# Performance work log

Hardware: AMD Instinct MI355X
Metric: run time of the kernel (lower is better)

The kernel has to match this reference:

```python
import jax, jax.numpy as jnp
import numpy as np

B, T, E, H = 2, 384, 768, 12
HD = E // H  # 64


def setup_inputs() -> dict:
    key = jax.random.key(0)
    ks = jax.random.split(key, 12)
    s = 0.02  # init scale
    inp = {
        "hidden_states": jax.random.normal(ks[0], (B, T, E), dtype=jnp.float32),
        # Linear weights stored as [in, out] so forward is x @ W + b
        "Wq": jax.random.normal(ks[1], (E, E), dtype=jnp.float32) * s,
        "bq": jnp.zeros((E,), dtype=jnp.float32),
        "Wk": jax.random.normal(ks[2], (E, E), dtype=jnp.float32) * s,
        "bk": jnp.zeros((E,), dtype=jnp.float32),
        "Wv": jax.random.normal(ks[3], (E, E), dtype=jnp.float32) * s,
        "bv": jnp.zeros((E,), dtype=jnp.float32),
        "Wo": jax.random.normal(ks[4], (E, E), dtype=jnp.float32) * s,
        "bo": jnp.zeros((E,), dtype=jnp.float32),
        # score_proj: Linear(head_dim, 1)
        "w_score": jax.random.normal(ks[5], (HD,), dtype=jnp.float32) * s,
        "b_score": jnp.zeros((1,), dtype=jnp.float32),
    }
    return inp


def reference(hidden_states, Wq, bq, Wk, bk, Wv, bv, Wo, bo, w_score, b_score):
    bsz, tgt_len, embed_dim = hidden_states.shape
    num_heads = H
    head_dim = embed_dim // num_heads

    def shape_heads(x):  # [B, L, E] -> [B, H, L, hd]
        return x.reshape(bsz, -1, num_heads, head_dim).transpose(0, 2, 1, 3)

    q = shape_heads(hidden_states @ Wq + bq)  # [B,H,T,hd]
    k = shape_heads(hidden_states @ Wk + bk)  # [B,H,S,hd]
    v = shape_heads(hidden_states @ Wv + bv)  # [B,H,S,hd]

    # additive (Bahdanau) score: score_proj(tanh(q_t + k_s)) -> [B,H,T,S]
    feat = jnp.tanh(q[:, :, :, None, :] + k[:, :, None, :, :])  # [B,H,T,S,hd]
    score = jnp.einsum("bhtsd,d->bhts", feat, w_score) + b_score[0]

    p_attn = jax.nn.softmax(score, axis=-1)                      # [B,H,T,S]
    attn = jnp.einsum("bhts,bhsd->bhtd", p_attn, v)              # [B,H,T,hd]

    attn = attn.transpose(0, 2, 1, 3).reshape(bsz, tgt_len, embed_dim)
    return attn @ Wo + bo
```

## Files before the change

kernel.cpp:

```cpp
#include <hip/hip_runtime.h>

#define Bc 2
#define Tc 384
#define Ec 768
#define Hc 12
#define HDc 64
#define TTc 8
#define SCc 64
#define NCHUNK (Tc / SCc)

typedef __attribute__((ext_vector_type(8))) short short8;
typedef __attribute__((ext_vector_type(4))) float f32x4;

#define CCONST 2.8853900817779268f

__device__ __forceinline__ float fexp2(float x) { return __builtin_amdgcn_exp2f(x); }
__device__ __forceinline__ float frcp(float x)  { return __builtin_amdgcn_rcpf(x); }

__device__ __forceinline__ unsigned short bf16_rne(float x) {
    unsigned u = __float_as_uint(x);
    u += 0x7fffu + ((u >> 16) & 1u);
    return (unsigned short)(u >> 16);
}
__device__ __forceinline__ float bf16_to_f(unsigned short h) {
    return __uint_as_float(((unsigned)h) << 16);
}

__global__ __launch_bounds__(256) void prep_kernel(
    const float* __restrict__ hs,
    const float* __restrict__ Wq, const float* __restrict__ Wk,
    const float* __restrict__ Wv, const float* __restrict__ Wo,
    unsigned short* __restrict__ hs_hi,
    unsigned short* __restrict__ wt_hi, unsigned short* __restrict__ wt_lo)
{
    const int tid = threadIdx.x;
    int id = blockIdx.x;
    if (id < 144) {
        int base = id * 4096 + tid * 16;
#pragma unroll
        for (int i = 0; i < 4; ++i) {
            float4 x = *reinterpret_cast<const float4*>(&hs[base + i * 4]);
            ushort4 hv;
            hv.x = bf16_rne(x.x);
            hv.y = bf16_rne(x.y);
            hv.z = bf16_rne(x.z);
            hv.w = bf16_rne(x.w);
            *reinterpret_cast<ushort4*>(&hs_hi[base + i * 4]) = hv;
        }
    } else {
        id -= 144;
        const int w = id / 144, t = id % 144;
        const int tr = t / 12, tc2 = t % 12;
        const float* W = (w == 0) ? Wq : (w == 1) ? Wk : (w == 2) ? Wv : Wo;
        unsigned short* TH = wt_hi + (size_t)w * Ec * Ec;
        unsigned short* TL = wt_lo + (size_t)w * Ec * Ec;

        __shared__ float tile[64][68];
        const int r = tid >> 2, c0 = (tid & 3) * 16;
#pragma unroll
        for (int i = 0; i < 4; ++i)
            *reinterpret_cast<float4*>(&tile[r][c0 + i * 4]) =
                *reinterpret_cast<const float4*>(&W[(tr * 64 + r) * Ec + tc2 * 64 + c0 + i * 4]);
        __syncthreads();
        const int n = tid >> 2, k0 = (tid & 3) * 4;
#pragma unroll
        for (int i = 0; i < 4; ++i) {
            int k = k0 + i * 16;
            float v0 = tile[k + 0][n], v1 = tile[k + 1][n];
            float v2 = tile[k + 2][n], v3 = tile[k + 3][n];
            ushort4 hv;
            hv.x = bf16_rne(v0);
            hv.y = bf16_rne(v1);
            hv.z = bf16_rne(v2);
            hv.w = bf16_rne(v3);
            size_t off = (size_t)(tc2 * 64 + n) * Ec + tr * 64 + k;
            *reinterpret_cast<ushort4*>(&TH[off]) = hv;
            if (w == 3) {
                ushort4 lv;
                lv.x = bf16_rne(v0 - bf16_to_f(hv.x));
                lv.y = bf16_rne(v1 - bf16_to_f(hv.y));
                lv.z = bf16_rne(v2 - bf16_to_f(hv.z));
                lv.w = bf16_rne(v3 - bf16_to_f(hv.w));
                *reinterpret_cast<ushort4*>(&TL[off]) = lv;
            }
        }
    }
}

__global__ __launch_bounds__(256) void gemm_qkv(
    const unsigned short* __restrict__ Ahi,
    const unsigned short* __restrict__ Bh0,
    const unsigned short* __restrict__ Bh1,
    const unsigned short* __restrict__ Bh2,
    const float* __restrict__ b0, const float* __restrict__ b1, const float* __restrict__ b2,
    float* __restrict__ C0, float* __restrict__ C1,
    unsigned short* __restrict__ Vt)
{
    const int z = blockIdx.z;
    const unsigned short* Bhi = (z == 0) ? Bh0 : (z == 1) ? Bh1 : Bh2;
    const float* bias = (z == 0) ? b0 : (z == 1) ? b1 : b2;

    __shared__ __align__(16) short sAh[64][72], sBh[64][72];

    const int tid = threadIdx.x;
    const int m0 = blockIdx.y * 64, n0 = blockIdx.x * 64;
    const int wave = tid >> 6, lane = tid & 63;
    const int wm = (wave >> 1) * 32, wn = (wave & 1) * 32;
    const int fr = lane & 15, fk = (lane >> 4) * 8;
    const int sr = tid >> 3, sg = (tid & 7) * 8;

    f32x4 zero = {0.f, 0.f, 0.f, 0.f};
    f32x4 acc[2][2];
    acc[0][0] = zero; acc[0][1] = zero; acc[1][0] = zero; acc[1][1] = zero;

    for (int kc = 0; kc < Ec; kc += 64) {
        int4 a0 = *reinterpret_cast<const int4*>(&Ahi[(size_t)(m0 + sr) * Ec + kc + sg]);
        int4 a1 = *reinterpret_cast<const int4*>(&Ahi[(size_t)(m0 + sr + 32) * Ec + kc + sg]);
        int4 w0 = *reinterpret_cast<const int4*>(&Bhi[(size_t)(n0 + sr) * Ec + kc + sg]);
        int4 w1 = *reinterpret_cast<const int4*>(&Bhi[(size_t)(n0 + sr + 32) * Ec + kc + sg]);
        __syncthreads();
        *reinterpret_cast<int4*>(&sAh[sr][sg])      = a0;
        *reinterpret_cast<int4*>(&sAh[sr + 32][sg]) = a1;
        *reinterpret_cast<int4*>(&sBh[sr][sg])      = w0;
        *reinterpret_cast<int4*>(&sBh[sr + 32][sg]) = w1;
        __syncthreads();

#pragma unroll
        for (int ks = 0; ks < 64; ks += 32) {
            short8 ah[2], bh[2];
#pragma unroll
            for (int mi = 0; mi < 2; ++mi)
                ah[mi] = *reinterpret_cast<const short8*>(&sAh[wm + mi * 16 + fr][ks + fk]);
#pragma unroll
            for (int ni = 0; ni < 2; ++ni)
                bh[ni] = *reinterpret_cast<const short8*>(&sBh[wn + ni * 16 + fr][ks + fk]);
#pragma unroll
            for (int mi = 0; mi < 2; ++mi)
#pragma unroll
                for (int ni = 0; ni < 2; ++ni)
                    acc[mi][ni] = __builtin_amdgcn_mfma_f32_16x16x32_bf16(ah[mi], bh[ni], acc[mi][ni], 0, 0, 0);
        }
        __syncthreads();
    }

    const int rbase = (lane >> 4) * 4;
#pragma unroll
    for (int ni = 0; ni < 2; ++ni) {
        const int cn = n0 + wn + ni * 16 + fr;
        const float bsv = bias[cn];
#pragma unroll
        for (int mi = 0; mi < 2; ++mi) {
            const int rm = m0 + wm + mi * 16 + rbase;
            if (z == 2) {
                const int bb = rm / Tc, ss = rm % Tc;
                const int hh = cn >> 6, dd = cn & 63;
                ushort4 pk;
                pk.x = bf16_rne(acc[mi][ni][0] + bsv);
                pk.y = bf16_rne(acc[mi][ni][1] + bsv);
                pk.z = bf16_rne(acc[mi][ni][2] + bsv);
                pk.w = bf16_rne(acc[mi][ni][3] + bsv);
                *reinterpret_cast<ushort4*>(
                    &Vt[((size_t)(bb * Hc + hh) * HDc + dd) * Tc + ss]) = pk;
            } else {
                float* C = (z == 0) ? C0 : C1;
#pragma unroll
                for (int rr = 0; rr < 4; ++rr)
                    C[(size_t)(rm + rr) * Ec + cn] = fexp2((acc[mi][ni][rr] + bsv) * CCONST);
            }
        }
    }
}

__global__ __launch_bounds__(256) void gemm_out(
    const unsigned short* __restrict__ Ahi, const unsigned short* __restrict__ Alo,
    const unsigned short* __restrict__ Bhi, const unsigned short* __restrict__ Blo,
    const float* __restrict__ bias_p,
    float* __restrict__ C0)
{
    __shared__ __align__(16) short sAh[64][72], sAl[64][72], sBh[64][72], sBl[64][72];

    const int tid = threadIdx.x;
    const int m0 = blockIdx.y * 64, n0 = blockIdx.x * 64;
    const int wave = tid >> 6, lane = tid & 63;
    const int wm = (wave >> 1) * 32, wn = (wave & 1) * 32;
    const int fr = lane & 15, fk = (lane >> 4) * 8;
    const int sr = tid >> 3, sg = (tid & 7) * 8;

    f32x4 zero = {0.f, 0.f, 0.f, 0.f};
    f32x4 acc[2][2];
    acc[0][0] = zero; acc[0][1] = zero; acc[1][0] = zero; acc[1][1] = zero;

    for (int kc = 0; kc < Ec; kc += 64) {
        int4 a0 = *reinterpret_cast<const int4*>(&Ahi[(size_t)(m0 + sr) * Ec + kc + sg]);
        int4 a1 = *reinterpret_cast<const int4*>(&Ahi[(size_t)(m0 + sr + 32) * Ec + kc + sg]);
        int4 a2 = *reinterpret_cast<const int4*>(&Alo[(size_t)(m0 + sr) * Ec + kc + sg]);
        int4 a3 = *reinterpret_cast<const int4*>(&Alo[(size_t)(m0 + sr + 32) * Ec + kc + sg]);
        int4 w0 = *reinterpret_cast<const int4*>(&Bhi[(size_t)(n0 + sr) * Ec + kc + sg]);
        int4 w1 = *reinterpret_cast<const int4*>(&Bhi[(size_t)(n0 + sr + 32) * Ec + kc + sg]);
        int4 w2 = *reinterpret_cast<const int4*>(&Blo[(size_t)(n0 + sr) * Ec + kc + sg]);
        int4 w3 = *reinterpret_cast<const int4*>(&Blo[(size_t)(n0 + sr + 32) * Ec + kc + sg]);
        __syncthreads();
        *reinterpret_cast<int4*>(&sAh[sr][sg])      = a0;
        *reinterpret_cast<int4*>(&sAh[sr + 32][sg]) = a1;
        *reinterpret_cast<int4*>(&sAl[sr][sg])      = a2;
        *reinterpret_cast<int4*>(&sAl[sr + 32][sg]) = a3;
        *reinterpret_cast<int4*>(&sBh[sr][sg])      = w0;
        *reinterpret_cast<int4*>(&sBh[sr + 32][sg]) = w1;
        *reinterpret_cast<int4*>(&sBl[sr][sg])      = w2;
        *reinterpret_cast<int4*>(&sBl[sr + 32][sg]) = w3;
        __syncthreads();

#pragma unroll
        for (int ks = 0; ks < 64; ks += 32) {
            short8 ah[2], al[2], bh[2], bl[2];
#pragma unroll
            for (int mi = 0; mi < 2; ++mi) {
                ah[mi] = *reinterpret_cast<const short8*>(&sAh[wm + mi * 16 + fr][ks + fk]);
                al[mi] = *reinterpret_cast<const short8*>(&sAl[wm + mi * 16 + fr][ks + fk]);
            }
#pragma unroll
            for (int ni = 0; ni < 2; ++ni) {
                bh[ni] = *reinterpret_cast<const short8*>(&sBh[wn + ni * 16 + fr][ks + fk]);
                bl[ni] = *reinterpret_cast<const short8*>(&sBl[wn + ni * 16 + fr][ks + fk]);
            }
#pragma unroll
            for (int mi = 0; mi < 2; ++mi)
#pragma unroll
                for (int ni = 0; ni < 2; ++ni) {
                    acc[mi][ni] = __builtin_amdgcn_mfma_f32_16x16x32_bf16(ah[mi], bh[ni], acc[mi][ni], 0, 0, 0);
                    acc[mi][ni] = __builtin_amdgcn_mfma_f32_16x16x32_bf16(ah[mi], bl[ni], acc[mi][ni], 0, 0, 0);
                    acc[mi][ni] = __builtin_amdgcn_mfma_f32_16x16x32_bf16(al[mi], bh[ni], acc[mi][ni], 0, 0, 0);
                }
        }
        __syncthreads();
    }

    const int rbase = (lane >> 4) * 4;
#pragma unroll
    for (int ni = 0; ni < 2; ++ni) {
        const int cn = n0 + wn + ni * 16 + fr;
        const float bsv = bias_p[cn];
#pragma unroll
        for (int mi = 0; mi < 2; ++mi) {
            const int rm = m0 + wm + mi * 16 + rbase;
#pragma unroll
            for (int rr = 0; rr < 4; ++rr)
                C0[(size_t)(rm + rr) * Ec + cn] = acc[mi][ni][rr] + bsv;
        }
    }
}

__global__ __launch_bounds__(256) void score_softmax_kernel(
    const float* __restrict__ EQ, const float* __restrict__ EK,
    const float* __restrict__ w_score,
    unsigned short* __restrict__ Pg, float* __restrict__ Rinv)
{
    const int bh = blockIdx.x;
    const int b = bh / Hc, h = bh % Hc;
    const int t0 = blockIdx.y * TTc;
    const int tid = threadIdx.x;
    const int wave = tid >> 6, lane = tid & 63;

    __shared__ float qs[TTc][HDc];
    __shared__ float kv[SCc][HDc + 4];
    __shared__ float wsh[HDc];

    {
        int r = tid >> 5, d2 = (tid & 31) << 1;
        float2 qv = *reinterpret_cast<const float2*>(
            &EQ[(size_t)(b * Tc + t0 + r) * Ec + h * HDc + d2]);
        qs[r][d2] = qv.x;
        qs[r][d2 + 1] = qv.y;
        if (tid < HDc) wsh[tid] = w_score[tid];
    }
    __syncthreads();

    const int ta = wave, tb = wave + 4;
    unsigned short* dstA = &Pg[((size_t)bh * Tc + t0 + ta) * Tc + lane];
    unsigned short* dstB = &Pg[((size_t)bh * Tc + t0 + tb) * Tc + lane];

    float sum0 = 0.f, sum1 = 0.f;

    for (int c = 0; c < NCHUNK; ++c) {
        const int s0 = c * SCc;
        if (c > 0) __syncthreads();
#pragma unroll
        for (int i = 0; i < 4; ++i) {
            int id = i * 256 + tid;
            int srr = id >> 4, d4 = (id & 15) << 2;
            float4 kvv = *reinterpret_cast<const float4*>(
                &EK[(size_t)(b * Tc + s0 + srr) * Ec + h * HDc + d4]);
            *reinterpret_cast<float4*>(&kv[srr][d4]) = kvv;
        }
        __syncthreads();
        float a0 = 0.f, a1 = 0.f;
#pragma unroll
        for (int d4 = 0; d4 < HDc; d4 += 4) {
            float4 w4 = *reinterpret_cast<const float4*>(&wsh[d4]);
            float4 qa = *reinterpret_cast<const float4*>(&qs[ta][d4]);
            float4 qb = *reinterpret_cast<const float4*>(&qs[tb][d4]);
            float4 k4 = *reinterpret_cast<const float4*>(&kv[lane][d4]);
            a0 = fmaf(w4.x, frcp(fmaf(qa.x, k4.x, 1.f)), a0);
            a0 = fmaf(w4.y, frcp(fmaf(qa.y, k4.y, 1.f)), a0);
            a0 = fmaf(w4.z, frcp(fmaf(qa.z, k4.z, 1.f)), a0);
            a0 = fmaf(w4.w, frcp(fmaf(qa.w, k4.w, 1.f)), a0);
            a1 = fmaf(w4.x, frcp(fmaf(qb.x, k4.x, 1.f)), a1);
            a1 = fmaf(w4.y, frcp(fmaf(qb.y, k4.y, 1.f)), a1);
            a1 = fmaf(w4.z, frcp(fmaf(qb.z, k4.z, 1.f)), a1);
            a1 = fmaf(w4.w, frcp(fmaf(qb.w, k4.w, 1.f)), a1);
        }
        float p0 = fexp2(-a0 * CCONST);
        float p1 = fexp2(-a1 * CCONST);
        dstA[s0] = bf16_rne(p0);
        dstB[s0] = bf16_rne(p1);
        sum0 += p0;
        sum1 += p1;
    }

#pragma unroll
    for (int off = 32; off > 0; off >>= 1) {
        sum0 += __shfl_xor(sum0, off, 64);
        sum1 += __shfl_xor(sum1, off, 64);
    }
    if (lane == 0) {
        Rinv[(size_t)bh * Tc + t0 + ta] = frcp(sum0);
        Rinv[(size_t)bh * Tc + t0 + tb] = frcp(sum1);
    }
}

__global__ __launch_bounds__(256) void pv_mfma(
    const unsigned short* __restrict__ Pg, const unsigned short* __restrict__ Vt,
    const float* __restrict__ Rinv,
    unsigned short* __restrict__ Ohi, unsigned short* __restrict__ Olo)
{
    const int bh = blockIdx.x;
    const int b = bh / Hc, h = bh % Hc;
    const int tt = blockIdx.y;
    const int tid = threadIdx.x;
    const int wave = tid >> 6, lane = tid & 63;
    const int fr = lane & 15, fk = (lane >> 4) * 8;

    const unsigned short* Pbase = Pg + ((size_t)bh * Tc + tt * 64 + wave * 16 + fr) * Tc + fk;
    const unsigned short* Vbase = Vt + (size_t)bh * HDc * Tc + fk;

    f32x4 zero = {0.f, 0.f, 0.f, 0.f};
    f32x4 acc[4];
    acc[0] = zero; acc[1] = zero; acc[2] = zero; acc[3] = zero;

    for (int ks = 0; ks < Tc; ks += 32) {
        short8 af = *reinterpret_cast<const short8*>(Pbase + ks);
#pragma unroll
        for (int ni = 0; ni < 4; ++ni) {
            short8 bf = *reinterpret_cast<const short8*>(
                Vbase + (size_t)(ni * 16 + fr) * Tc + ks);
            acc[ni] = __builtin_amdgcn_mfma_f32_16x16x32_bf16(af, bf, acc[ni], 0, 0, 0);
        }
    }

    const int rbase = (lane >> 4) * 4;
    float rv[4];
#pragma unroll
    for (int rr = 0; rr < 4; ++rr)
        rv[rr] = Rinv[(size_t)bh * Tc + tt * 64 + wave * 16 + rbase + rr];

#pragma unroll
    for (int ni = 0; ni < 4; ++ni) {
#pragma unroll
        for (int rr = 0; rr < 4; ++rr) {
            int t_out = tt * 64 + wave * 16 + rbase + rr;
            float x = acc[ni][rr] * rv[rr];
            unsigned short hb = bf16_rne(x);
            unsigned short lb = bf16_rne(x - bf16_to_f(hb));
            size_t idx = (size_t)(b * Tc + t_out) * Ec + h * HDc + ni * 16 + fr;
            Ohi[idx] = hb;
            Olo[idx] = lb;
        }
    }
}

extern "C" void kernel_launch(void* const* d_in, const int* in_sizes, int n_in,
                              void* d_out, int out_size, void* d_ws, size_t ws_size,
                              hipStream_t stream) {
    const float* hs  = (const float*)d_in[0];
    const float* Wq  = (const float*)d_in[1];
    const float* bq  = (const float*)d_in[2];
    const float* Wk  = (const float*)d_in[3];
    const float* bk  = (const float*)d_in[4];
    const float* Wv  = (const float*)d_in[5];
    const float* bv  = (const float*)d_in[6];
    const float* Wo  = (const float*)d_in[7];
    const float* bo  = (const float*)d_in[8];
    const float* wsc = (const float*)d_in[9];
    float* out = (float*)d_out;

    const size_t MAT = (size_t)(Bc * Tc) * Ec;
    const size_t PSZ = (size_t)Bc * Hc * Tc * Tc;
    float* EQw = (float*)d_ws;
    float* EKw = EQw + MAT;
    float* Rinv = EKw + MAT;
    unsigned short* Vt    = (unsigned short*)(Rinv + (size_t)Bc * Hc * Tc);
    unsigned short* Pgb   = Vt + MAT;
    unsigned short* HS_HI = Pgb + PSZ;
    unsigned short* HS_LO = HS_HI + MAT;
    unsigned short* WT_HI = HS_LO + MAT;
    unsigned short* WT_LO = WT_HI + 4 * MAT;

    prep_kernel<<<720, 256, 0, stream>>>(hs, Wq, Wk, Wv, Wo, HS_HI, WT_HI, WT_LO);

    gemm_qkv<<<dim3(Ec / 64, (Bc * Tc) / 64, 3), 256, 0, stream>>>(
        HS_HI,
        WT_HI + 0 * MAT, WT_HI + 1 * MAT, WT_HI + 2 * MAT,
        bq, bk, bv, EQw, EKw, Vt);

    score_softmax_kernel<<<dim3(Bc * Hc, Tc / TTc), 256, 0, stream>>>(
        EQw, EKw, wsc, Pgb, Rinv);

    pv_mfma<<<dim3(Bc * Hc, Tc / 64), 256, 0, stream>>>(Pgb, Vt, Rinv, HS_HI, HS_LO);

    gemm_out<<<dim3(Ec / 64, (Bc * Tc) / 64, 1), 256, 0, stream>>>(
        HS_HI, HS_LO,
        WT_HI + 3 * MAT, WT_LO + 3 * MAT,
        bo, out);
}
```

Before: 79.76 us.

## Restructure score kernel: one key per thread in registers, 384 threads per block

The score/softmax kernel now launches 384 threads per block. Each thread owns one key position and keeps that key's 64-wide row in registers, then loops over the block's 8 query rows, reading q and w_score directly from global memory (wave-uniform, so likely scalar or broadcast loads). This removes the shared-memory staging of K chunks and the per-chunk barriers. Row sums are reduced per wave and combined across the 6 waves through a small shared array. In exchange, register pressure rises (64 floats of K per thread) and every query read now goes to global or L1 instead of LDS.

```diff
diff --git a/kernel.cpp b/kernel.cpp
--- a/kernel.cpp
+++ b/kernel.cpp
@@ -6,8 +6,6 @@
 #define Hc 12
 #define HDc 64
 #define TTc 8
-#define SCc 64
-#define NCHUNK (Tc / SCc)
 
 typedef __attribute__((ext_vector_type(8))) short short8;
 typedef __attribute__((ext_vector_type(4))) float f32x4;
@@ -250,7 +248,7 @@
     }
 }
 
-__global__ __launch_bounds__(256) void score_softmax_kernel(
+__global__ __launch_bounds__(384) void score_softmax_kernel(
     const float* __restrict__ EQ, const float* __restrict__ EK,
     const float* __restrict__ w_score,
     unsigned short* __restrict__ Pg, float* __restrict__ Rinv)
@@ -260,71 +258,53 @@
     const int t0 = blockIdx.y * TTc;
     const int tid = threadIdx.x;
     const int wave = tid >> 6, lane = tid & 63;
-
-    __shared__ float qs[TTc][HDc];
-    __shared__ float kv[SCc][HDc + 4];
-    __shared__ float wsh[HDc];
-
-    {
-        int r = tid >> 5, d2 = (tid & 31) << 1;
-        float2 qv = *reinterpret_cast<const float2*>(
-            &EQ[(size_t)(b * Tc + t0 + r) * Ec + h * HDc + d2]);
-        qs[r][d2] = qv.x;
-        qs[r][d2 + 1] = qv.y;
-        if (tid < HDc) wsh[tid] = w_score[tid];
+    const int s = wave * 64 + lane;
+
+    __shared__ float psum[TTc][8];
+
+    const float* ek = EK + (size_t)(b * Tc + s) * Ec + h * HDc;
+    float4 kr0  = *reinterpret_cast<const float4*>(ek + 0);
+    float4 kr1  = *reinterpret_cast<const float4*>(ek + 4);
+    float4 kr2  = *reinterpret_cast<const float4*>(ek + 8);
+    float4 kr3  = *reinterpret_cast<const float4*>(ek + 12);
+    float4 kr4  = *reinterpret_cast<const float4*>(ek + 16);
+    float4 kr5  = *reinterpret_cast<const float4*>(ek + 20);
+    float4 kr6  = *reinterpret_cast<const float4*>(ek + 24);
+    float4 kr7  = *reinterpret_cast<const float4*>(ek + 28);
+    float4 kr8  = *reinterpret_cast<const float4*>(ek + 32);
+    float4 kr9  = *reinterpret_cast<const float4*>(ek + 36);
+    float4 kr10 = *reinterpret_cast<const float4*>(ek + 40);
+    float4 kr11 = *reinterpret_cast<const float4*>(ek + 44);
+    float4 kr12 = *reinterpret_cast<const float4*>(ek + 48);
+    float4 kr13 = *reinterpret_cast<const float4*>(ek + 52);
+    float4 kr14 = *reinterpret_cast<const float4*>(ek + 56);
+    float4 kr15 = *reinterpret_cast<const float4*>(ek + 60);
+
+    for (int t = 0; t < TTc; ++t) {
+        const float* qr = EQ + (size_t)(b * Tc + t0 + t) * Ec + h * HDc;
+        float a = 0.f;
+#define SIG4(KR, D0)                                                          \
+        a = fmaf(w_score[D0 + 0], frcp(fmaf(qr[D0 + 0], KR.x, 1.f)), a);      \
+        a = fmaf(w_score[D0 + 1], frcp(fmaf(qr[D0 + 1], KR.y, 1.f)), a);      \
+        a = fmaf(w_score[D0 + 2], frcp(fmaf(qr[D0 + 2], KR.z, 1.f)), a);      \
+        a = fmaf(w_score[D0 + 3], frcp(fmaf(qr[D0 + 3], KR.w, 1.f)), a);
+        SIG4(kr0, 0)   SIG4(kr1, 4)   SIG4(kr2, 8)   SIG4(kr3, 12)
+        SIG4(kr4, 16)  SIG4(kr5, 20)  SIG4(kr6, 24)  SIG4(kr7, 28)
+        SIG4(kr8, 32)  SIG4(kr9, 36)  SIG4(kr10, 40) SIG4(kr11, 44)
+        SIG4(kr12, 48) SIG4(kr13, 52) SIG4(kr14, 56) SIG4(kr15, 60)
+#undef SIG4
+        float p = fexp2(-a * CCONST);
+        Pg[((size_t)bh * Tc + t0 + t) * Tc + s] = bf16_rne(p);
+        float sum = p;
+#pragma unroll
+        for (int off = 32; off > 0; off >>= 1) sum += __shfl_xor(sum, off, 64);
+        if (lane == 0) psum[t][wave] = sum;
     }
     __syncthreads();
-
-    const int ta = wave, tb = wave + 4;
-    unsigned short* dstA = &Pg[((size_t)bh * Tc + t0 + ta) * Tc + lane];
-    unsigned short* dstB = &Pg[((size_t)bh * Tc + t0 + tb) * Tc + lane];
-
-    float sum0 = 0.f, sum1 = 0.f;
-
-    for (int c = 0; c < NCHUNK; ++c) {
-        const int s0 = c * SCc;
-        if (c > 0) __syncthreads();
-#pragma unroll
-        for (int i = 0; i < 4; ++i) {
-            int id = i * 256 + tid;
-            int srr = id >> 4, d4 = (id & 15) << 2;
-            float4 kvv = *reinterpret_cast<const float4*>(
-                &EK[(size_t)(b * Tc + s0 + srr) * Ec + h * HDc + d4]);
-            *reinterpret_cast<float4*>(&kv[srr][d4]) = kvv;
-        }
-        __syncthreads();
-        float a0 = 0.f, a1 = 0.f;
-#pragma unroll
-        for (int d4 = 0; d4 < HDc; d4 += 4) {
-            float4 w4 = *reinterpret_cast<const float4*>(&wsh[d4]);
-            float4 qa = *reinterpret_cast<const float4*>(&qs[ta][d4]);
-            float4 qb = *reinterpret_cast<const float4*>(&qs[tb][d4]);
-            float4 k4 = *reinterpret_cast<const float4*>(&kv[lane][d4]);
-            a0 = fmaf(w4.x, frcp(fmaf(qa.x, k4.x, 1.f)), a0);
-            a0 = fmaf(w4.y, frcp(fmaf(qa.y, k4.y, 1.f)), a0);
-            a0 = fmaf(w4.z, frcp(fmaf(qa.z, k4.z, 1.f)), a0);
-            a0 = fmaf(w4.w, frcp(fmaf(qa.w, k4.w, 1.f)), a0);
-            a1 = fmaf(w4.x, frcp(fmaf(qb.x, k4.x, 1.f)), a1);
-            a1 = fmaf(w4.y, frcp(fmaf(qb.y, k4.y, 1.f)), a1);
-            a1 = fmaf(w4.z, frcp(fmaf(qb.z, k4.z, 1.f)), a1);
-            a1 = fmaf(w4.w, frcp(fmaf(qb.w, k4.w, 1.f)), a1);
-        }
-        float p0 = fexp2(-a0 * CCONST);
-        float p1 = fexp2(-a1 * CCONST);
-        dstA[s0] = bf16_rne(p0);
-        dstB[s0] = bf16_rne(p1);
-        sum0 += p0;
-        sum1 += p1;
-    }
-
-#pragma unroll
-    for (int off = 32; off > 0; off >>= 1) {
-        sum0 += __shfl_xor(sum0, off, 64);
-        sum1 += __shfl_xor(sum1, off, 64);
-    }
-    if (lane == 0) {
-        Rinv[(size_t)bh * Tc + t0 + ta] = frcp(sum0);
-        Rinv[(size_t)bh * Tc + t0 + tb] = frcp(sum1);
+    if (tid < TTc) {
+        float s6 = psum[tid][0] + psum[tid][1] + psum[tid][2] +
+                   psum[tid][3] + psum[tid][4] + psum[tid][5];
+        Rinv[(size_t)bh * Tc + t0 + tid] = frcp(s6);
     }
 }
 
@@ -412,7 +392,7 @@
         WT_HI + 0 * MAT, WT_HI + 1 * MAT, WT_HI + 2 * MAT,
         bq, bk, bv, EQw, EKw, Vt);
 
-    score_softmax_kernel<<<dim3(Bc * Hc, Tc / TTc), 256, 0, stream>>>(
+    score_softmax_kernel<<<dim3(Bc * Hc, Tc / TTc), 384, 0, stream>>>(
         EQw, EKw, wsc, Pgb, Rinv);
 
     pv_mfma<<<dim3(Bc * Hc, Tc / 64), 256, 0, stream>>>(Pgb, Vt, Rinv, HS_HI, HS_LO);
```

Result: slower. 91.14 us (+14.3%).

## Split score kernel over key dimension and combine partial softmax sums in PV

Applied to the files above, without the earlier changes.

The score/softmax kernel grid gains a z dimension that splits the key axis into two halves. Each block writes partial row sums instead of reciprocals, and the PV kernel adds the two partials and takes the reciprocal. This doubles the block count (1152 to 2304) to raise occupancy and parallelism on the tanh-heavy score stage, at the cost of loading Q twice. It also drops the shared-memory copy of w_score and reads it directly from global memory, relying on uniform scalar loads.

```diff
diff --git a/kernel.cpp b/kernel.cpp
--- a/kernel.cpp
+++ b/kernel.cpp
@@ -7,7 +7,10 @@
 #define HDc 64
 #define TTc 8
 #define SCc 64
-#define NCHUNK (Tc / SCc)
+#define SSPLIT 2
+#define SHALF (Tc / SSPLIT)
+#define NCHUNK (SHALF / SCc)
+#define BHT (Bc * Hc * Tc)
 
 typedef __attribute__((ext_vector_type(8))) short short8;
 typedef __attribute__((ext_vector_type(4))) float f32x4;
@@ -253,17 +256,17 @@
 __global__ __launch_bounds__(256) void score_softmax_kernel(
     const float* __restrict__ EQ, const float* __restrict__ EK,
     const float* __restrict__ w_score,
-    unsigned short* __restrict__ Pg, float* __restrict__ Rinv)
+    unsigned short* __restrict__ Pg, float* __restrict__ Rpart)
 {
     const int bh = blockIdx.x;
     const int b = bh / Hc, h = bh % Hc;
     const int t0 = blockIdx.y * TTc;
+    const int sbase = blockIdx.z * SHALF;
     const int tid = threadIdx.x;
     const int wave = tid >> 6, lane = tid & 63;
 
     __shared__ float qs[TTc][HDc];
     __shared__ float kv[SCc][HDc + 4];
-    __shared__ float wsh[HDc];
 
     {
         int r = tid >> 5, d2 = (tid & 31) << 1;
@@ -271,18 +274,17 @@
             &EQ[(size_t)(b * Tc + t0 + r) * Ec + h * HDc + d2]);
         qs[r][d2] = qv.x;
         qs[r][d2 + 1] = qv.y;
-        if (tid < HDc) wsh[tid] = w_score[tid];
     }
     __syncthreads();
 
     const int ta = wave, tb = wave + 4;
-    unsigned short* dstA = &Pg[((size_t)bh * Tc + t0 + ta) * Tc + lane];
-    unsigned short* dstB = &Pg[((size_t)bh * Tc + t0 + tb) * Tc + lane];
+    unsigned short* dstA = &Pg[((size_t)bh * Tc + t0 + ta) * Tc + sbase + lane];
+    unsigned short* dstB = &Pg[((size_t)bh * Tc + t0 + tb) * Tc + sbase + lane];
 
     float sum0 = 0.f, sum1 = 0.f;
 
     for (int c = 0; c < NCHUNK; ++c) {
-        const int s0 = c * SCc;
+        const int s0 = sbase + c * SCc;
         if (c > 0) __syncthreads();
 #pragma unroll
         for (int i = 0; i < 4; ++i) {
@@ -296,23 +298,22 @@
         float a0 = 0.f, a1 = 0.f;
 #pragma unroll
         for (int d4 = 0; d4 < HDc; d4 += 4) {
-            float4 w4 = *reinterpret_cast<const float4*>(&wsh[d4]);
+            float4 k4 = *reinterpret_cast<const float4*>(&kv[lane][d4]);
             float4 qa = *reinterpret_cast<const float4*>(&qs[ta][d4]);
             float4 qb = *reinterpret_cast<const float4*>(&qs[tb][d4]);
-            float4 k4 = *reinterpret_cast<const float4*>(&kv[lane][d4]);
-            a0 = fmaf(w4.x, frcp(fmaf(qa.x, k4.x, 1.f)), a0);
-            a0 = fmaf(w4.y, frcp(fmaf(qa.y, k4.y, 1.f)), a0);
-            a0 = fmaf(w4.z, frcp(fmaf(qa.z, k4.z, 1.f)), a0);
-            a0 = fmaf(w4.w, frcp(fmaf(qa.w, k4.w, 1.f)), a0);
-            a1 = fmaf(w4.x, frcp(fmaf(qb.x, k4.x, 1.f)), a1);
-            a1 = fmaf(w4.y, frcp(fmaf(qb.y, k4.y, 1.f)), a1);
-            a1 = fmaf(w4.z, frcp(fmaf(qb.z, k4.z, 1.f)), a1);
-            a1 = fmaf(w4.w, frcp(fmaf(qb.w, k4.w, 1.f)), a1);
+            a0 = fmaf(w_score[d4 + 0], frcp(fmaf(qa.x, k4.x, 1.f)), a0);
+            a0 = fmaf(w_score[d4 + 1], frcp(fmaf(qa.y, k4.y, 1.f)), a0);
+            a0 = fmaf(w_score[d4 + 2], frcp(fmaf(qa.z, k4.z, 1.f)), a0);
+            a0 = fmaf(w_score[d4 + 3], frcp(fmaf(qa.w, k4.w, 1.f)), a0);
+            a1 = fmaf(w_score[d4 + 0], frcp(fmaf(qb.x, k4.x, 1.f)), a1);
+            a1 = fmaf(w_score[d4 + 1], frcp(fmaf(qb.y, k4.y, 1.f)), a1);
+            a1 = fmaf(w_score[d4 + 2], frcp(fmaf(qb.z, k4.z, 1.f)), a1);
+            a1 = fmaf(w_score[d4 + 3], frcp(fmaf(qb.w, k4.w, 1.f)), a1);
         }
         float p0 = fexp2(-a0 * CCONST);
         float p1 = fexp2(-a1 * CCONST);
-        dstA[s0] = bf16_rne(p0);
-        dstB[s0] = bf16_rne(p1);
+        dstA[c * SCc] = bf16_rne(p0);
+        dstB[c * SCc] = bf16_rne(p1);
         sum0 += p0;
         sum1 += p1;
     }
@@ -323,14 +324,14 @@
         sum1 += __shfl_xor(sum1, off, 64);
     }
     if (lane == 0) {
-        Rinv[(size_t)bh * Tc + t0 + ta] = frcp(sum0);
-        Rinv[(size_t)bh * Tc + t0 + tb] = frcp(sum1);
+        Rpart[(size_t)blockIdx.z * BHT + bh * Tc + t0 + ta] = sum0;
+        Rpart[(size_t)blockIdx.z * BHT + bh * Tc + t0 + tb] = sum1;
     }
 }
 
 __global__ __launch_bounds__(256) void pv_mfma(
     const unsigned short* __restrict__ Pg, const unsigned short* __restrict__ Vt,
-    const float* __restrict__ Rinv,
+    const float* __restrict__ Rpart,
     unsigned short* __restrict__ Ohi, unsigned short* __restrict__ Olo)
 {
     const int bh = blockIdx.x;
@@ -360,8 +361,10 @@
     const int rbase = (lane >> 4) * 4;
     float rv[4];
 #pragma unroll
-    for (int rr = 0; rr < 4; ++rr)
-        rv[rr] = Rinv[(size_t)bh * Tc + tt * 64 + wave * 16 + rbase + rr];
+    for (int rr = 0; rr < 4; ++rr) {
+        size_t ridx = (size_t)bh * Tc + tt * 64 + wave * 16 + rbase + rr;
+        rv[rr] = frcp(Rpart[ridx] + Rpart[ridx + BHT]);
+    }
 
 #pragma unroll
     for (int ni = 0; ni < 4; ++ni) {
@@ -397,8 +400,8 @@
     const size_t PSZ = (size_t)Bc * Hc * Tc * Tc;
     float* EQw = (float*)d_ws;
     float* EKw = EQw + MAT;
-    float* Rinv = EKw + MAT;
-    unsigned short* Vt    = (unsigned short*)(Rinv + (size_t)Bc * Hc * Tc);
+    float* Rpart = EKw + MAT;
+    unsigned short* Vt    = (unsigned short*)(Rpart + 2 * (size_t)BHT);
     unsigned short* Pgb   = Vt + MAT;
     unsigned short* HS_HI = Pgb + PSZ;
     unsigned short* HS_LO = HS_HI + MAT;
@@ -412,10 +415,10 @@
         WT_HI + 0 * MAT, WT_HI + 1 * MAT, WT_HI + 2 * MAT,
         bq, bk, bv, EQw, EKw, Vt);
 
-    score_softmax_kernel<<<dim3(Bc * Hc, Tc / TTc), 256, 0, stream>>>(
-        EQw, EKw, wsc, Pgb, Rinv);
-
-    pv_mfma<<<dim3(Bc * Hc, Tc / 64), 256, 0, stream>>>(Pgb, Vt, Rinv, HS_HI, HS_LO);
+    score_softmax_kernel<<<dim3(Bc * Hc, Tc / TTc, SSPLIT), 256, 0, stream>>>(
+        EQw, EKw, wsc, Pgb, Rpart);
+
+    pv_mfma<<<dim3(Bc * Hc, Tc / 64), 256, 0, stream>>>(Pgb, Vt, Rpart, HS_HI, HS_LO);
 
     gemm_out<<<dim3(Ec / 64, (Bc * Tc) / 64, 1), 256, 0, stream>>>(
         HS_HI, HS_LO,
```

Measured after the change: 75.50 us. 5.3% less time.
